# Kernel tuning notes

Measured on AMD Instinct MI355X. Metric: run time of the kernel, lower is better.

The kernel has to match this reference:

```python
import jax, jax.numpy as jnp
import numpy as np

D_GNN, D_MODEL = 512, 2048
B, T = 4, 4096
EPS = 1e-5


def layer_norm(x, gamma, beta):
    mu = jnp.mean(x, axis=-1, keepdims=True)
    var = jnp.mean(jnp.square(x - mu), axis=-1, keepdims=True)
    return (x - mu) * jax.lax.rsqrt(var + EPS) * gamma + beta


def setup_inputs() -> dict:
    key = jax.random.key(0)
    ks = jax.random.split(key, 10)
    s_proj = 1.0 / np.sqrt(D_GNN)
    s_mod = 1.0 / np.sqrt(D_MODEL)
    s_gate = 1.0 / np.sqrt(2 * D_MODEL)
    return {
        "h_llm": jax.random.normal(ks[0], (B, T, D_MODEL), jnp.float32),
        "h_change": jax.random.normal(ks[1], (B, D_GNN), jnp.float32),
        # h_change_proj: Linear(d_gnn -> d_model)
        "w_proj": jax.random.uniform(ks[2], (D_MODEL, D_GNN), jnp.float32, -s_proj, s_proj),
        "b_proj": jnp.zeros((D_MODEL,), jnp.float32),
        "g1": jnp.ones((D_MODEL,), jnp.float32),
        "b1": jnp.zeros((D_MODEL,), jnp.float32),
        # MHA value / output projections (q,k are mathematically irrelevant: kv_len==1 -> softmax==1)
        "w_v": jax.random.uniform(ks[3], (D_MODEL, D_MODEL), jnp.float32, -s_mod, s_mod),
        "b_v": jnp.zeros((D_MODEL,), jnp.float32),
        "w_o": jax.random.uniform(ks[4], (D_MODEL, D_MODEL), jnp.float32, -s_mod, s_mod),
        "b_o": jnp.zeros((D_MODEL,), jnp.float32),
        "g2": jnp.ones((D_MODEL,), jnp.float32),
        "b2": jnp.zeros((D_MODEL,), jnp.float32),
        # fusion gate: Linear(2*d_model -> d_model) + sigmoid
        "w_gate": jax.random.uniform(ks[5], (D_MODEL, 2 * D_MODEL), jnp.float32, -s_gate, s_gate),
        "b_gate": jnp.zeros((D_MODEL,), jnp.float32),
        "g3": jnp.ones((D_MODEL,), jnp.float32),
        "b3": jnp.zeros((D_MODEL,), jnp.float32),
    }


def reference(h_llm, h_change, w_proj, b_proj, g1, b1, w_v, b_v, w_o, b_o,
              g2, b2, w_gate, b_gate, g3, b3):
    # project GNN feature to d_model, then LayerNorm  -> (B, D)
    hc = layer_norm(h_change @ w_proj.T + b_proj, g1, b1)
    # cross-attention with kv_len == 1: softmax over a single key is identically 1,
    # so attn_output == out_proj(value_proj(hc)), broadcast over T. Dropout is eval (identity).
    attn = (hc @ w_v.T + b_v) @ w_o.T + b_o                 # (B, D)
    attn_out = layer_norm(h_llm + attn[:, None, :], g2, b2)  # (B, T, D)
    # gated residual fusion: gate = sigmoid(W [h_llm ; attn_out] + b)
    wg_l, wg_a = w_gate[:, :D_MODEL], w_gate[:, D_MODEL:]
    gate = jax.nn.sigmoid(h_llm @ wg_l.T + attn_out @ wg_a.T + b_gate)
    fused = gate * attn_out + (1.0 - gate) * h_llm
    return layer_norm(fused, g3, b3)
```

## Files before the change

kernel.cpp:

```cpp
#include <hip/hip_runtime.h>
#include <hip/hip_bf16.h>
#include <cstdint>
#include <cstddef>

#define DM 2048
#define DG 512
#define NBATCH 4
#define NT 4096
#define NM (NBATCH*NT)
#define KC (2*DM)
#define LN_EPS 1e-5f
#define NTILES (KC/64)
#define SCL_A 16.0f
#define SCL_B 8192.0f
#define DESCALE (1.0f/131072.0f)
#define INV_SCL_A 0.0625f

typedef __bf16 bf16;
typedef bf16 bf16x8 __attribute__((ext_vector_type(8)));
typedef float f32x4 __attribute__((ext_vector_type(4)));
typedef int   i32x4 __attribute__((ext_vector_type(4)));
typedef char  i8x8  __attribute__((ext_vector_type(8)));
typedef unsigned char u8x8 __attribute__((ext_vector_type(8)));

#define AS1 __attribute__((address_space(1)))
#define AS3 __attribute__((address_space(3)))

__device__ __forceinline__ char q8(float x, float s) {
    int v = (int)rintf(x * s);
    v = v > 127 ? 127 : (v < -127 ? -127 : v);
    return (char)v;
}

__device__ __forceinline__ void block_reduce_2(float& s, float& s2) {
#pragma unroll
    for (int off = 32; off; off >>= 1) {
        s  += __shfl_down(s, off);
        s2 += __shfl_down(s2, off);
    }
    __shared__ float sm[8];
    const int wid = threadIdx.x >> 6, lane = threadIdx.x & 63;
    if (lane == 0) { sm[wid] = s; sm[4 + wid] = s2; }
    __syncthreads();
    s  = sm[0] + sm[1] + sm[2] + sm[3];
    s2 = sm[4] + sm[5] + sm[6] + sm[7];
}

__global__ void k_pack_dot1(const float* __restrict__ wg, int8_t* __restrict__ wqb,
                            const float* __restrict__ X, const float* __restrict__ W,
                            const float* __restrict__ bias, float* __restrict__ out) {
    if (blockIdx.x >= 512) {
        const int i = (blockIdx.x - 512) * 256 + threadIdx.x;
        const f32x4* s = (const f32x4*)wg + (size_t)i * 2;
        f32x4 a = s[0], b = s[1];
        i8x8 o;
#pragma unroll
        for (int q = 0; q < 4; q++) { o[q] = q8(a[q], SCL_B); o[4+q] = q8(b[q], SCL_B); }
        *((i8x8*)wqb + i) = o;
        return;
    }
    const int lane = threadIdx.x & 63;
    const int wid  = threadIdx.x >> 6;
    const int j = blockIdx.x * 4 + wid;
    const f32x4* Wr = (const f32x4*)(W + (size_t)j * DG);
    float acc[NBATCH] = {0.f, 0.f, 0.f, 0.f};
    constexpr int C = DG / 4 / 64;
#pragma unroll
    for (int i = 0; i < C; i++) {
        f32x4 wv = Wr[lane + 64 * i];
#pragma unroll
        for (int b = 0; b < NBATCH; b++) {
            f32x4 xv = ((const f32x4*)(X + (size_t)b * DG))[lane + 64 * i];
            acc[b] += wv[0]*xv[0] + wv[1]*xv[1] + wv[2]*xv[2] + wv[3]*xv[3];
        }
    }
#pragma unroll
    for (int off = 32; off; off >>= 1)
#pragma unroll
        for (int b = 0; b < NBATCH; b++) acc[b] += __shfl_down(acc[b], off);
    if (lane == 0) {
        const float bb = bias[j];
#pragma unroll
        for (int b = 0; b < NBATCH; b++) out[(size_t)b * DM + j] = acc[b] + bb;
    }
}

template<int K>
__global__ void k_dot(const float* __restrict__ X, const float* __restrict__ W,
                      const float* __restrict__ bias, float* __restrict__ out) {
    const int lane = threadIdx.x & 63;
    const int wid  = threadIdx.x >> 6;
    const int j = blockIdx.x * 4 + wid;
    const f32x4* Wr = (const f32x4*)(W + (size_t)j * K);
    float acc[NBATCH] = {0.f, 0.f, 0.f, 0.f};
    constexpr int C = K / 4 / 64;
#pragma unroll
    for (int i = 0; i < C; i++) {
        f32x4 wv = Wr[lane + 64 * i];
#pragma unroll
        for (int b = 0; b < NBATCH; b++) {
            f32x4 xv = ((const f32x4*)(X + (size_t)b * K))[lane + 64 * i];
            acc[b] += wv[0]*xv[0] + wv[1]*xv[1] + wv[2]*xv[2] + wv[3]*xv[3];
        }
    }
#pragma unroll
    for (int off = 32; off; off >>= 1)
#pragma unroll
        for (int b = 0; b < NBATCH; b++) acc[b] += __shfl_down(acc[b], off);
    if (lane == 0) {
        const float bb = bias[j];
#pragma unroll
        for (int b = 0; b < NBATCH; b++) out[(size_t)b * DM + j] = acc[b] + bb;
    }
}

__global__ void k_ln_small(const float* __restrict__ in, const float* __restrict__ g,
                           const float* __restrict__ bt, float* __restrict__ out) {
    const int row = blockIdx.x;
    const int tid = threadIdx.x;
    const f32x4* ir = (const f32x4*)(in + (size_t)row * DM);
    f32x4 v0 = ir[tid], v1 = ir[tid + 256];
    float s  = v0[0]+v0[1]+v0[2]+v0[3] + v1[0]+v1[1]+v1[2]+v1[3];
    float s2 = v0[0]*v0[0]+v0[1]*v0[1]+v0[2]*v0[2]+v0[3]*v0[3]
             + v1[0]*v1[0]+v1[1]*v1[1]+v1[2]*v1[2]+v1[3]*v1[3];
    block_reduce_2(s, s2);
    const float mu = s * (1.0f / DM);
    const float r  = rsqrtf(s2 * (1.0f / DM) - mu * mu + LN_EPS);
    f32x4 g0 = ((const f32x4*)g)[tid],  g1v = ((const f32x4*)g)[tid + 256];
    f32x4 b0 = ((const f32x4*)bt)[tid], b1v = ((const f32x4*)bt)[tid + 256];
    f32x4 o0 = (v0 - mu) * r * g0 + b0;
    f32x4 o1 = (v1 - mu) * r * g1v + b1v;
    f32x4* orow = (f32x4*)(out + (size_t)row * DM);
    orow[tid] = o0; orow[tid + 256] = o1;
}

__global__ void k_stats_pack(const float* __restrict__ h, const float* __restrict__ attnv,
                             const float* __restrict__ g2, const float* __restrict__ b2,
                             int8_t* __restrict__ Aq,
                             float* __restrict__ muA, float* __restrict__ rA) {
    const int m = blockIdx.x;
    const int b = m >> 12;
    const int tid = threadIdx.x;
    const f32x4* hr = (const f32x4*)(h + (size_t)m * DM);
    const f32x4* ar = (const f32x4*)(attnv + (size_t)b * DM);
    f32x4 h0 = hr[2*tid], h1 = hr[2*tid + 1];
    f32x4 a0 = ar[2*tid], a1 = ar[2*tid + 1];
    f32x4 x0 = h0 + a0, x1 = h1 + a1;
    float s  = x0[0]+x0[1]+x0[2]+x0[3] + x1[0]+x1[1]+x1[2]+x1[3];
    float s2 = x0[0]*x0[0]+x0[1]*x0[1]+x0[2]*x0[2]+x0[3]*x0[3]
             + x1[0]*x1[0]+x1[1]*x1[1]+x1[2]*x1[2]+x1[3]*x1[3];
    block_reduce_2(s, s2);
    const float mu = s * (1.0f / DM);
    const float r  = rsqrtf(s2 * (1.0f / DM) - mu * mu + LN_EPS);
    if (tid == 0) { muA[m] = mu; rA[m] = r; }
    f32x4 gg0 = ((const f32x4*)g2)[2*tid], gg1 = ((const f32x4*)g2)[2*tid + 1];
    f32x4 bb0 = ((const f32x4*)b2)[2*tid], bb1 = ((const f32x4*)b2)[2*tid + 1];
    f32x4 ao0 = (x0 - mu) * r * gg0 + bb0;
    f32x4 ao1 = (x1 - mu) * r * gg1 + bb1;
    i8x8 qh, qa;
#pragma unroll
    for (int q = 0; q < 4; q++) {
        qh[q] = q8(h0[q], SCL_A);  qh[4+q] = q8(h1[q], SCL_A);
        qa[q] = q8(ao0[q], SCL_A); qa[4+q] = q8(ao1[q], SCL_A);
    }
    *(i8x8*)(Aq + (size_t)m * KC + 8*tid) = qh;
    *(i8x8*)(Aq + (size_t)m * KC + DM + 8*tid) = qa;
}

#define MF(a,b,c) __builtin_amdgcn_mfma_i32_16x16x64_i8(a,b,c,0,0,0)
#define SCHED0() __builtin_amdgcn_sched_barrier(0)
#define BAR()  { SCHED0(); asm volatile("s_barrier" ::: "memory"); SCHED0(); }
#define VM(n)  { asm volatile("s_waitcnt vmcnt(" #n ")" ::: "memory"); SCHED0(); }
#define LGKM(n) { asm volatile("s_waitcnt lgkmcnt(" #n ")" ::: "memory"); SCHED0(); }

__global__ __launch_bounds__(512, 2) void k_gemm256(const int8_t* __restrict__ A, const int8_t* __restrict__ Bw,
                                                    const float* __restrict__ bgate, uint8_t* __restrict__ gq) {
    __shared__ __align__(128) char smem[98304];
    const int tid  = threadIdx.x;
    const int lane = tid & 63;
    const int wid  = tid >> 6;
    const int wm   = wid >> 2, wn = wid & 3;

    const int swz = (blockIdx.x & 7) * 64 + (blockIdx.x >> 3);
    const int bm = (swz >> 3) << 8;
    const int bn = (swz & 7) << 8;

    const int r_local = tid >> 2;
    const int sc = (tid & 3) ^ (r_local & 3);
    const int8_t* Abase = A  + (size_t)(bm + r_local) * KC + sc*16;
    const int8_t* Bbase = Bw + (size_t)(bn + r_local) * KC + sc*16;
    const int ldsW = wid << 10;

#define STAGEAU(O, u, kt) __builtin_amdgcn_global_load_lds( \
        (const AS1 void*)(Abase + (size_t)(u)*128*KC + (kt)*64), \
        (AS3 void*)(smem + (O) + (u)*8192 + ldsW), 16, 0, 0)
#define STAGEBU(O, u, kt) __builtin_amdgcn_global_load_lds( \
        (const AS1 void*)(Bbase + (size_t)(u)*128*KC + (kt)*64), \
        (AS3 void*)(smem + (O) + 16384 + (u)*8192 + ldsW), 16, 0, 0)

    const int co   = ((lane >> 4) ^ (lane & 3)) << 4;
    const int aoff = (wm*128 + (lane & 15)) * 64 + co;
    const int boff = 16384 + (wn*64 + (lane & 15)) * 64 + co;

#define DSA(O, m) (*(const i32x4*)(smem + (O) + aoff + (m)*1024))
#define DSB(O, n) (*(const i32x4*)(smem + (O) + boff + (n)*1024))

    i32x4 acc[8][4] = {};
    i32x4 a0,a1,a2,a3,a4,a5,a6,a7;
    i32x4 bc0,bc1,bc2,bc3, bn0,bn1,bn2,bn3;

#define MM4(AR, B0,B1,B2,B3, M) { \
    __builtin_amdgcn_s_setprio(1); \
    acc[M][0] = MF(AR, B0, acc[M][0]); \
    acc[M][1] = MF(AR, B1, acc[M][1]); \
    acc[M][2] = MF(AR, B2, acc[M][2]); \
    acc[M][3] = MF(AR, B3, acc[M][3]); \
    __builtin_amdgcn_s_setprio(0); SCHED0(); }

#define TFULL(T_, O0_, O1_, O2_, C0,C1,C2,C3, N0,N1,N2,N3, G2_) { \
    if (G2_) { STAGEAU(O0_ ,0,0); }  }

#undef TFULL
#define TFULL(T_, O0_, O1_, O2_, C0,C1,C2,C3, N0,N1,N2,N3, G2_) { \
    if (G2_) { STAGEAU(O2_, 0, (T_)+2); } \
    a2 = DSA(O0_, 2); SCHED0(); LGKM(2); MM4(a0, C0,C1,C2,C3, 0); \
    if (G2_) { STAGEAU(O2_, 1, (T_)+2); } \
    a3 = DSA(O0_, 3); SCHED0(); LGKM(2); MM4(a1, C0,C1,C2,C3, 1); \
    if (G2_) { STAGEBU(O2_, 0, (T_)+2); } \
    a4 = DSA(O0_, 4); N0 = DSB(O1_, 0); SCHED0(); LGKM(3); MM4(a2, C0,C1,C2,C3, 2); \
    if (G2_) { STAGEBU(O2_, 1, (T_)+2); } \
    a5 = DSA(O0_, 5); N1 = DSB(O1_, 1); SCHED0(); LGKM(4); MM4(a3, C0,C1,C2,C3, 3); \
    a6 = DSA(O0_, 6); N2 = DSB(O1_, 2); SCHED0(); LGKM(5); MM4(a4, C0,C1,C2,C3, 4); \
    a7 = DSA(O0_, 7); N3 = DSB(O1_, 3); SCHED0(); LGKM(5); MM4(a5, C0,C1,C2,C3, 5); \
    a0 = DSA(O1_, 0); SCHED0(); LGKM(4); MM4(a6, C0,C1,C2,C3, 6); \
    a1 = DSA(O1_, 1); SCHED0(); LGKM(3); MM4(a7, C0,C1,C2,C3, 7); \
    VM(0); \
    BAR(); }

#define TTAIL(O0_, C0,C1,C2,C3) { \
    a2 = DSA(O0_, 2); SCHED0(); LGKM(2); MM4(a0, C0,C1,C2,C3, 0); \
    a3 = DSA(O0_, 3); SCHED0(); LGKM(2); MM4(a1, C0,C1,C2,C3, 1); \
    a4 = DSA(O0_, 4); SCHED0(); LGKM(2); MM4(a2, C0,C1,C2,C3, 2); \
    a5 = DSA(O0_, 5); SCHED0(); LGKM(2); MM4(a3, C0,C1,C2,C3, 3); \
    a6 = DSA(O0_, 6); SCHED0(); LGKM(2); MM4(a4, C0,C1,C2,C3, 4); \
    a7 = DSA(O0_, 7); SCHED0(); LGKM(2); MM4(a5, C0,C1,C2,C3, 5); \
    LGKM(1); MM4(a6, C0,C1,C2,C3, 6); \
    LGKM(0); MM4(a7, C0,C1,C2,C3, 7); }

#define ROT() { int t_ = o0; o0 = o1; o1 = o2; o2 = t_; }

    int o0 = 0, o1 = 32768, o2 = 65536;

    STAGEAU(0, 0, 0); STAGEAU(0, 1, 0); STAGEBU(0, 0, 0); STAGEBU(0, 1, 0);
    STAGEAU(32768, 0, 1); STAGEAU(32768, 1, 1); STAGEBU(32768, 0, 1); STAGEBU(32768, 1, 1);
    VM(0);
    BAR();
    bc0 = DSB(0, 0); bc1 = DSB(0, 1); bc2 = DSB(0, 2); bc3 = DSB(0, 3);
    a0 = DSA(0, 0); a1 = DSA(0, 1); SCHED0();

    for (int it = 0; it < 31; ++it) {
        const int T = 2 * it;
        TFULL(T,   o0, o1, o2, bc0,bc1,bc2,bc3, bn0,bn1,bn2,bn3, true); ROT();
        TFULL(T+1, o0, o1, o2, bn0,bn1,bn2,bn3, bc0,bc1,bc2,bc3, true); ROT();
    }
    TFULL(62, o0, o1, o2, bc0,bc1,bc2,bc3, bn0,bn1,bn2,bn3, false); ROT();
    TTAIL(o0, bn0,bn1,bn2,bn3);

#pragma unroll
    for (int n = 0; n < 4; n++) {
        const int col = bn + wn*64 + n*16 + (lane & 15);
        const float bg = bgate[col];
#pragma unroll
        for (int m = 0; m < 8; m++) {
            const int row = bm + wm*128 + m*16 + ((lane >> 4) << 2);
#pragma unroll
            for (int r = 0; r < 4; r++) {
                const float z = (float)acc[m][n][r] * DESCALE + bg;
                const float gate = 1.0f / (1.0f + __expf(-z));
                gq[(size_t)(row + r) * DM + col] = (uint8_t)(int)rintf(gate * 255.0f);
            }
        }
    }
}

__global__ void k_epilogue(const int8_t* __restrict__ Aq, const uint8_t* __restrict__ gq,
                           const float* __restrict__ attnv, const float* __restrict__ muA,
                           const float* __restrict__ rA,
                           const float* __restrict__ g2, const float* __restrict__ b2,
                           const float* __restrict__ g3, const float* __restrict__ b3,
                           float* __restrict__ out) {
    const int m = blockIdx.x;
    const int b = m >> 12;
    const int tid = threadIdx.x;
    i8x8 qh = *(const i8x8*)(Aq + (size_t)m * KC + 8*tid);
    f32x4 h0, h1;
#pragma unroll
    for (int q = 0; q < 4; q++) { h0[q] = (float)qh[q] * INV_SCL_A; h1[q] = (float)qh[4+q] * INV_SCL_A; }
    const f32x4* ar = (const f32x4*)(attnv + (size_t)b * DM);
    f32x4 a0 = ar[2*tid], a1 = ar[2*tid + 1];
    const float mu = muA[m];
    const float r  = rA[m];
    f32x4 gg0 = ((const f32x4*)g2)[2*tid], gg1 = ((const f32x4*)g2)[2*tid + 1];
    f32x4 bb0 = ((const f32x4*)b2)[2*tid], bb1 = ((const f32x4*)b2)[2*tid + 1];
    f32x4 ao0 = (h0 + a0 - mu) * r * gg0 + bb0;
    f32x4 ao1 = (h1 + a1 - mu) * r * gg1 + bb1;
    u8x8 qv = *(const u8x8*)(gq + (size_t)m * DM + 8*tid);
    f32x4 gt0, gt1;
#pragma unroll
    for (int q = 0; q < 4; q++) {
        gt0[q] = (float)qv[q]   * (1.0f / 255.0f);
        gt1[q] = (float)qv[4+q] * (1.0f / 255.0f);
    }
    f32x4 f0 = h0 + gt0 * (ao0 - h0);
    f32x4 f1 = h1 + gt1 * (ao1 - h1);
    float s  = f0[0]+f0[1]+f0[2]+f0[3] + f1[0]+f1[1]+f1[2]+f1[3];
    float s2 = f0[0]*f0[0]+f0[1]*f0[1]+f0[2]*f0[2]+f0[3]*f0[3]
             + f1[0]*f1[0]+f1[1]*f1[1]+f1[2]*f1[2]+f1[3]*f1[3];
    block_reduce_2(s, s2);
    const float mu3 = s * (1.0f / DM);
    const float r3  = rsqrtf(s2 * (1.0f / DM) - mu3 * mu3 + LN_EPS);
    f32x4 g30 = ((const f32x4*)g3)[2*tid], g31 = ((const f32x4*)g3)[2*tid + 1];
    f32x4 b30 = ((const f32x4*)b3)[2*tid], b31 = ((const f32x4*)b3)[2*tid + 1];
    f32x4 o0 = (f0 - mu3) * r3 * g30 + b30;
    f32x4 o1 = (f1 - mu3) * r3 * g31 + b31;
    f32x4* orow = (f32x4*)(out + (size_t)m * DM);
    orow[2*tid] = o0; orow[2*tid + 1] = o1;
}

extern "C" void kernel_launch(void* const* d_in, const int* in_sizes, int n_in,
                              void* d_out, int out_size, void* d_ws, size_t ws_size,
                              hipStream_t stream) {
    const float* h_llm    = (const float*)d_in[0];
    const float* h_change = (const float*)d_in[1];
    const float* w_proj   = (const float*)d_in[2];
    const float* b_proj   = (const float*)d_in[3];
    const float* g1       = (const float*)d_in[4];
    const float* b1       = (const float*)d_in[5];
    const float* w_v      = (const float*)d_in[6];
    const float* b_v      = (const float*)d_in[7];
    const float* w_o      = (const float*)d_in[8];
    const float* b_o      = (const float*)d_in[9];
    const float* g2       = (const float*)d_in[10];
    const float* b2       = (const float*)d_in[11];
    const float* w_gate   = (const float*)d_in[12];
    const float* b_gate   = (const float*)d_in[13];
    const float* g3       = (const float*)d_in[14];
    const float* b3       = (const float*)d_in[15];
    float* out = (float*)d_out;

    char* ws = (char*)d_ws;
    int8_t* Aq  = (int8_t*)ws; ws += (size_t)NM * KC;
    int8_t* wqb = (int8_t*)ws; ws += (size_t)DM * KC;
    uint8_t* gq = (uint8_t*)ws; ws += (size_t)NM * DM;
    float* muA = (float*)ws;  ws += (size_t)NM * 4;
    float* rA  = (float*)ws;  ws += (size_t)NM * 4;
    float* raw1 = (float*)ws; ws += (size_t)NBATCH * DM * 4;
    float* hc   = (float*)ws; ws += (size_t)NBATCH * DM * 4;
    float* raw2 = (float*)ws; ws += (size_t)NBATCH * DM * 4;
    float* attnv= (float*)ws; ws += (size_t)NBATCH * DM * 4;

    k_pack_dot1<<<4608, 256, 0, stream>>>(w_gate, wqb, h_change, w_proj, b_proj, raw1);
    k_ln_small<<<NBATCH, 256, 0, stream>>>(raw1, g1, b1, hc);
    k_dot<DM><<<DM / 4, 256, 0, stream>>>(hc, w_v, b_v, raw2);
    k_dot<DM><<<DM / 4, 256, 0, stream>>>(raw2, w_o, b_o, attnv);
    k_stats_pack<<<NM, 256, 0, stream>>>(h_llm, attnv, g2, b2, Aq, muA, rA);
    k_gemm256<<<512, 512, 0, stream>>>(Aq, wqb, b_gate, gq);
    k_epilogue<<<NM, 256, 0, stream>>>(Aq, gq, attnv, muA, rA, g2, b2, g3, b3, out);
}
```

Before: 252.1 us.

## Replace triple-buffered swizzled LDS pipeline with simple double-buffered loop

Restructures the int8 GEMM main loop from a three-stage LDS ring with cross-tile register prefetch of A/B fragments to a two-buffer scheme. Each tile now loads all fragments from LDS first, then issues the next tile's global-to-LDS copies. It also removes the XOR swizzle on LDS staging and reads and cuts shared memory from 96KB to 64KB. This simplifies the code and lowers LDS footprint, but risks LDS bank conflicts and less overlap between loads and MFMA work.

```diff
diff --git a/kernel.cpp b/kernel.cpp
--- a/kernel.cpp
+++ b/kernel.cpp
@@ -175,7 +175,7 @@
 
 __global__ __launch_bounds__(512, 2) void k_gemm256(const int8_t* __restrict__ A, const int8_t* __restrict__ Bw,
                                                     const float* __restrict__ bgate, uint8_t* __restrict__ gq) {
-    __shared__ __align__(128) char smem[98304];
+    __shared__ __align__(128) char smem[65536];
     const int tid  = threadIdx.x;
     const int lane = tid & 63;
     const int wid  = tid >> 6;
@@ -185,86 +185,63 @@
     const int bm = (swz >> 3) << 8;
     const int bn = (swz & 7) << 8;
 
-    const int r_local = tid >> 2;
-    const int sc = (tid & 3) ^ (r_local & 3);
-    const int8_t* Abase = A  + (size_t)(bm + r_local) * KC + sc*16;
-    const int8_t* Bbase = Bw + (size_t)(bn + r_local) * KC + sc*16;
+    const int8_t* Abase = A  + (size_t)(bm + (tid >> 2)) * KC + (tid & 3) * 16;
+    const int8_t* Bbase = Bw + (size_t)(bn + (tid >> 2)) * KC + (tid & 3) * 16;
     const int ldsW = wid << 10;
 
-#define STAGEAU(O, u, kt) __builtin_amdgcn_global_load_lds( \
+#define STAGEA(O, u, kt) __builtin_amdgcn_global_load_lds( \
         (const AS1 void*)(Abase + (size_t)(u)*128*KC + (kt)*64), \
         (AS3 void*)(smem + (O) + (u)*8192 + ldsW), 16, 0, 0)
-#define STAGEBU(O, u, kt) __builtin_amdgcn_global_load_lds( \
+#define STAGEB(O, u, kt) __builtin_amdgcn_global_load_lds( \
         (const AS1 void*)(Bbase + (size_t)(u)*128*KC + (kt)*64), \
         (AS3 void*)(smem + (O) + 16384 + (u)*8192 + ldsW), 16, 0, 0)
 
-    const int co   = ((lane >> 4) ^ (lane & 3)) << 4;
-    const int aoff = (wm*128 + (lane & 15)) * 64 + co;
-    const int boff = 16384 + (wn*64 + (lane & 15)) * 64 + co;
+    const int aoff = (wm*128 + (lane & 15)) * 64 + ((lane >> 4) << 4);
+    const int boff = 16384 + (wn*64 + (lane & 15)) * 64 + ((lane >> 4) << 4);
 
 #define DSA(O, m) (*(const i32x4*)(smem + (O) + aoff + (m)*1024))
 #define DSB(O, n) (*(const i32x4*)(smem + (O) + boff + (n)*1024))
 
     i32x4 acc[8][4] = {};
-    i32x4 a0,a1,a2,a3,a4,a5,a6,a7;
-    i32x4 bc0,bc1,bc2,bc3, bn0,bn1,bn2,bn3;
-
-#define MM4(AR, B0,B1,B2,B3, M) { \
+    i32x4 a0,a1,a2,a3,a4,a5,a6,a7, b0,b1,b2,b3;
+
+#define MM4(AR, M) { \
     __builtin_amdgcn_s_setprio(1); \
-    acc[M][0] = MF(AR, B0, acc[M][0]); \
-    acc[M][1] = MF(AR, B1, acc[M][1]); \
-    acc[M][2] = MF(AR, B2, acc[M][2]); \
-    acc[M][3] = MF(AR, B3, acc[M][3]); \
+    acc[M][0] = MF(AR, b0, acc[M][0]); \
+    acc[M][1] = MF(AR, b1, acc[M][1]); \
+    acc[M][2] = MF(AR, b2, acc[M][2]); \
+    acc[M][3] = MF(AR, b3, acc[M][3]); \
     __builtin_amdgcn_s_setprio(0); SCHED0(); }
 
-#define TFULL(T_, O0_, O1_, O2_, C0,C1,C2,C3, N0,N1,N2,N3, G2_) { \
-    if (G2_) { STAGEAU(O0_ ,0,0); }  }
-
-#undef TFULL
-#define TFULL(T_, O0_, O1_, O2_, C0,C1,C2,C3, N0,N1,N2,N3, G2_) { \
-    if (G2_) { STAGEAU(O2_, 0, (T_)+2); } \
-    a2 = DSA(O0_, 2); SCHED0(); LGKM(2); MM4(a0, C0,C1,C2,C3, 0); \
-    if (G2_) { STAGEAU(O2_, 1, (T_)+2); } \
-    a3 = DSA(O0_, 3); SCHED0(); LGKM(2); MM4(a1, C0,C1,C2,C3, 1); \
-    if (G2_) { STAGEBU(O2_, 0, (T_)+2); } \
-    a4 = DSA(O0_, 4); N0 = DSB(O1_, 0); SCHED0(); LGKM(3); MM4(a2, C0,C1,C2,C3, 2); \
-    if (G2_) { STAGEBU(O2_, 1, (T_)+2); } \
-    a5 = DSA(O0_, 5); N1 = DSB(O1_, 1); SCHED0(); LGKM(4); MM4(a3, C0,C1,C2,C3, 3); \
-    a6 = DSA(O0_, 6); N2 = DSB(O1_, 2); SCHED0(); LGKM(5); MM4(a4, C0,C1,C2,C3, 4); \
-    a7 = DSA(O0_, 7); N3 = DSB(O1_, 3); SCHED0(); LGKM(5); MM4(a5, C0,C1,C2,C3, 5); \
-    a0 = DSA(O1_, 0); SCHED0(); LGKM(4); MM4(a6, C0,C1,C2,C3, 6); \
-    a1 = DSA(O1_, 1); SCHED0(); LGKM(3); MM4(a7, C0,C1,C2,C3, 7); \
-    VM(0); \
-    BAR(); }
-
-#define TTAIL(O0_, C0,C1,C2,C3) { \
-    a2 = DSA(O0_, 2); SCHED0(); LGKM(2); MM4(a0, C0,C1,C2,C3, 0); \
-    a3 = DSA(O0_, 3); SCHED0(); LGKM(2); MM4(a1, C0,C1,C2,C3, 1); \
-    a4 = DSA(O0_, 4); SCHED0(); LGKM(2); MM4(a2, C0,C1,C2,C3, 2); \
-    a5 = DSA(O0_, 5); SCHED0(); LGKM(2); MM4(a3, C0,C1,C2,C3, 3); \
-    a6 = DSA(O0_, 6); SCHED0(); LGKM(2); MM4(a4, C0,C1,C2,C3, 4); \
-    a7 = DSA(O0_, 7); SCHED0(); LGKM(2); MM4(a5, C0,C1,C2,C3, 5); \
-    LGKM(1); MM4(a6, C0,C1,C2,C3, 6); \
-    LGKM(0); MM4(a7, C0,C1,C2,C3, 7); }
-
-#define ROT() { int t_ = o0; o0 = o1; o1 = o2; o2 = t_; }
-
-    int o0 = 0, o1 = 32768, o2 = 65536;
-
-    STAGEAU(0, 0, 0); STAGEAU(0, 1, 0); STAGEBU(0, 0, 0); STAGEBU(0, 1, 0);
-    STAGEAU(32768, 0, 1); STAGEAU(32768, 1, 1); STAGEBU(32768, 0, 1); STAGEBU(32768, 1, 1);
+#define TILE_BODY(TT, O_, NO_) { \
+    const bool g = (TT) < NTILES - 1; \
+    b0 = DSB(O_,0); b1 = DSB(O_,1); b2 = DSB(O_,2); b3 = DSB(O_,3); \
+    a0 = DSA(O_,0); a1 = DSA(O_,1); a2 = DSA(O_,2); a3 = DSA(O_,3); \
+    a4 = DSA(O_,4); a5 = DSA(O_,5); a6 = DSA(O_,6); a7 = DSA(O_,7); SCHED0(); \
+    LGKM(7); MM4(a0, 0); \
+    if (g) { STAGEA(NO_, 0, (TT)+1); } \
+    LGKM(6); MM4(a1, 1); \
+    if (g) { STAGEA(NO_, 1, (TT)+1); } \
+    LGKM(5); MM4(a2, 2); \
+    if (g) { STAGEB(NO_, 0, (TT)+1); } \
+    LGKM(4); MM4(a3, 3); \
+    if (g) { STAGEB(NO_, 1, (TT)+1); } \
+    LGKM(3); MM4(a4, 4); \
+    LGKM(2); MM4(a5, 5); \
+    LGKM(1); MM4(a6, 6); \
+    LGKM(0); MM4(a7, 7); \
+    if (g) { VM(0); } \
+    BAR(); \
+}
+
+    STAGEA(0, 0, 0); STAGEA(0, 1, 0); STAGEB(0, 0, 0); STAGEB(0, 1, 0);
     VM(0);
     BAR();
-    bc0 = DSB(0, 0); bc1 = DSB(0, 1); bc2 = DSB(0, 2); bc3 = DSB(0, 3);
-    a0 = DSA(0, 0); a1 = DSA(0, 1); SCHED0();
-
-    for (int it = 0; it < 31; ++it) {
-        const int T = 2 * it;
-        TFULL(T,   o0, o1, o2, bc0,bc1,bc2,bc3, bn0,bn1,bn2,bn3, true); ROT();
-        TFULL(T+1, o0, o1, o2, bn0,bn1,bn2,bn3, bc0,bc1,bc2,bc3, true); ROT();
-    }
-    TFULL(62, o0, o1, o2, bc0,bc1,bc2,bc3, bn0,bn1,bn2,bn3, false); ROT();
-    TTAIL(o0, bn0,bn1,bn2,bn3);
+
+    for (int T = 0; T < NTILES; T += 2) {
+        TILE_BODY(T,   0,     32768);
+        TILE_BODY(T+1, 32768, 0);
+    }
 
 #pragma unroll
     for (int n = 0; n < 4; n++) {
```

Measured after the change: 266.2 us. 1.06x slower.
